# Optimization experiments

Measured on AMD Instinct MI355X. Metric: run time of the kernel, lower is better.

## Reference

```python
import jax, jax.numpy as jnp
import numpy as np

N = 100000
E = 3200000
IN_C, HID_C, OUT_C = 128, 128, 64


def setup_inputs() -> dict:
    key = jax.random.key(0)
    k_x, k_e, k_w1, k_w2 = jax.random.split(key, 4)
    x = jax.random.normal(k_x, (N, IN_C), dtype=jnp.float32)
    edge_index = jax.random.randint(k_e, (2, E), 0, N, dtype=jnp.int64)
    # GCNConv uses Glorot-init weight [in, out] and zero bias
    W1 = jax.random.normal(k_w1, (IN_C, HID_C), dtype=jnp.float32) * (1.0 / np.sqrt(IN_C))
    b1 = jnp.zeros((HID_C,), dtype=jnp.float32)
    W2 = jax.random.normal(k_w2, (HID_C, OUT_C), dtype=jnp.float32) * (1.0 / np.sqrt(HID_C))
    b2 = jnp.zeros((OUT_C,), dtype=jnp.float32)
    return {"x": x, "edge_index": edge_index, "W1": W1, "b1": b1, "W2": W2, "b2": b2}


def _gcn_norm(edge_index, n_nodes):
    """Add self-loops and compute symmetric normalization coefficients."""
    loop = jnp.arange(n_nodes, dtype=edge_index.dtype)
    src = jnp.concatenate([edge_index[0], loop])  # [E+N]
    dst = jnp.concatenate([edge_index[1], loop])  # [E+N]
    ones = jnp.ones(src.shape[0], dtype=jnp.float32)
    deg = jax.ops.segment_sum(ones, dst, num_segments=n_nodes)  # in-degree w/ self loops
    dinv = jnp.where(deg > 0, jax.lax.rsqrt(deg), 0.0)
    norm = dinv[src] * dinv[dst]  # [E+N]
    return src, dst, norm


def _gcn_conv(x, W, b, src, dst, norm, n_nodes):
    h = x @ W                                   # [N, out] dense transform first (PyG order)
    msg = norm[:, None] * h[src]                # gather + scale  [E+N, out]
    out = jax.ops.segment_sum(msg, dst, num_segments=n_nodes)  # scatter-add
    return out + b


def reference(x, edge_index, W1, b1, W2, b2):
    src, dst, norm = _gcn_norm(edge_index, N)
    h = _gcn_conv(x, W1, b1, src, dst, norm, N)
    h = jax.nn.relu(h)
    out = _gcn_conv(h, W2, b2, src, dst, norm, N)
    return out
```

## Files before the change

kernel.cpp:

```cpp
#include <hip/hip_runtime.h>

typedef unsigned int u32;
typedef unsigned short u16;
typedef unsigned long long u64;
typedef __bf16 bf16x8 __attribute__((ext_vector_type(8)));
typedef float floatx4 __attribute__((ext_vector_type(4)));
typedef float floatx2 __attribute__((ext_vector_type(2)));
typedef u32 u32x2 __attribute__((ext_vector_type(2)));
typedef u32 u32x4 __attribute__((ext_vector_type(4)));


__device__ __forceinline__ u16 f2bf(float f) {
  u32 u = __float_as_uint(f);
  u += 0x7fffu + ((u >> 16) & 1u);
  return (u16)(u >> 16);
}
__device__ __forceinline__ float bflo(u32 v) { return __uint_as_float(v << 16); }
__device__ __forceinline__ float bfhi(u32 v) { return __uint_as_float(v & 0xffff0000u); }
__device__ __forceinline__ floatx2 bf2(u32 v) {
  floatx2 r; r.x = bflo(v); r.y = bfhi(v); return r;
}

#define SLICE_SH 10
#define SL (1 << SLICE_SH)
#define MAXNS 128
#define NBBIN 1280

__device__ __forceinline__ void gemm1_body(const float* __restrict__ X,
                                           const float* __restrict__ W,
                                           u16* __restrict__ Y, int nrows,
                                           int bid, u16* Wt) {
  constexpr int K = 128, OUT = 128, NT = 8, LDW = 136;
  int tid = threadIdx.x;
  for (int idx = tid; idx < K * OUT; idx += 256) {
    int k = idx >> 7, n = idx & 127;
    Wt[n * LDW + k] = f2bf(W[idx]);
  }
  __syncthreads();
  int lane = tid & 63, wave = tid >> 6;
  int quad = lane >> 4, low = lane & 15;
  int mBase = bid * 64 + wave * 16;
  int m = mBase + low;
  int ml = (m < nrows) ? m : (nrows - 1);
  floatx4 acc[NT];
#pragma unroll
  for (int i = 0; i < NT; i++) acc[i] = (floatx4)0.0f;
#pragma unroll
  for (int kb = 0; kb < 4; kb++) {
    int k0 = kb * 32 + quad * 8;
    floatx4 p0 = *(const floatx4*)(X + (size_t)ml * K + k0);
    floatx4 p1 = *(const floatx4*)(X + (size_t)ml * K + k0 + 4);
    union { bf16x8 v; u16 s[8]; } au;
#pragma unroll
    for (int j = 0; j < 4; j++) { au.s[j] = f2bf(p0[j]); au.s[4 + j] = f2bf(p1[j]); }
#pragma unroll
    for (int nt = 0; nt < NT; nt++) {
      bf16x8 b = *(const bf16x8*)(&Wt[(nt * 16 + low) * LDW + k0]);
      acc[nt] = __builtin_amdgcn_mfma_f32_16x16x32_bf16(au.v, b, acc[nt], 0, 0, 0);
    }
  }
#pragma unroll
  for (int nt = 0; nt < NT; nt++) {
    int col = nt * 16 + low;
#pragma unroll
    for (int r = 0; r < 4; r++) {
      int row = mBase + quad * 4 + r;
      if (row < nrows) Y[(size_t)row * OUT + col] = f2bf(acc[nt][r]);
    }
  }
}

__device__ __forceinline__ void bin_body(const int* __restrict__ ei,
                                         int* __restrict__ scur,
                                         u64* __restrict__ stA, u64* __restrict__ stB,
                                         int splitS, int cap, int e, int ns,
                                         int bid, int* hist, int* curs) {
  int per = (e + NBBIN - 1) / NBBIN;
  int e0 = bid * per;
  int e1 = e0 + per; if (e1 > e) e1 = e;
  for (int t = threadIdx.x; t < ns; t += 256) hist[t] = 0;
  __syncthreads();
  for (int i = e0 + threadIdx.x; i < e1; i += 256) {
    int d = ei[e + i];
    atomicAdd(&hist[d >> SLICE_SH], 1);
  }
  __syncthreads();
  for (int t = threadIdx.x; t < ns; t += 256)
    curs[t] = atomicAdd(&scur[t], hist[t]);
  __syncthreads();
  int i = e0 + threadIdx.x;
  for (; i + 768 < e1; i += 1024) {
    int d[4], s[4], pos[4];
#pragma unroll
    for (int p = 0; p < 4; p++) {
      int ii = i + 256 * p;
      s[p] = ei[ii]; d[p] = ei[e + ii];
    }
#pragma unroll
    for (int p = 0; p < 4; p++) pos[p] = atomicAdd(&curs[d[p] >> SLICE_SH], 1);
#pragma unroll
    for (int p = 0; p < 4; p++) {
      int sl = d[p] >> SLICE_SH;
      u64* st = (sl < splitS) ? stA + (size_t)sl * cap : stB + (size_t)(sl - splitS) * cap;
      st[pos[p]] = ((u64)(u32)d[p] << 32) | (u32)s[p];
    }
  }
  for (; i < e1; i += 256) {
    int s = ei[i], d = ei[e + i];
    int sl = d >> SLICE_SH;
    u64* st = (sl < splitS) ? stA + (size_t)sl * cap : stB + (size_t)(sl - splitS) * cap;
    st[atomicAdd(&curs[sl], 1)] = ((u64)(u32)d << 32) | (u32)s;
  }
}

__global__ __launch_bounds__(256) void gemm1_bin(const float* __restrict__ X,
                                                 const float* __restrict__ W1,
                                                 u16* __restrict__ Y, int nrows, int nbGemm,
                                                 const int* __restrict__ ei,
                                                 int* __restrict__ scur,
                                                 u64* __restrict__ stA, u64* __restrict__ stB,
                                                 int splitS, int cap, int e, int ns) {
  __shared__ __attribute__((aligned(16))) char smbuf[128 * 136 * 2];
  int id = blockIdx.x;
  int small = (NBBIN < nbGemm) ? NBBIN : nbGemm;
  int isBin, bid;
  if (id < 2 * small) { isBin = !(id & 1); bid = id >> 1; }
  else { bid = small + (id - 2 * small); isBin = (NBBIN > nbGemm); }
  if (isBin) {
    int* hist = (int*)smbuf;
    int* curs = hist + MAXNS;
    bin_body(ei, scur, stA, stB, splitS, cap, e, ns, bid, hist, curs);
  } else {
    gemm1_body(X, W1, Y, nrows, bid, (u16*)smbuf);
  }
}

__global__ __launch_bounds__(1024) void fill_slice3(const u64* __restrict__ stA,
                                                    const u64* __restrict__ stB,
                                                    const int* __restrict__ scur,
                                                    int* __restrict__ rp,
                                                    float* __restrict__ dinv,
                                                    int* __restrict__ csr,
                                                    int splitS, int cap, int n, int ns) {
  __shared__ int cnt[SL];
  __shared__ int part[SL];
  __shared__ int sb[MAXNS];
  const int s = blockIdx.x;
  const int base = s << SLICE_SH;
  const int tid = threadIdx.x;
  cnt[tid] = 0;
  if (tid < MAXNS) sb[tid] = (tid < ns) ? scur[tid] : 0;
  __syncthreads();
  for (int off = 1; off < MAXNS; off <<= 1) {
    int v = 0;
    if (tid < MAXNS && tid >= off) v = sb[tid - off];
    __syncthreads();
    if (tid < MAXNS) sb[tid] += v;
    __syncthreads();
  }
  const int csrLo = s ? sb[s - 1] : 0;
  const int m = sb[s] - csrLo;
  if (s == ns - 1 && tid == 0) rp[n] = sb[ns - 1];
  const u64* st = (s < splitS) ? stA + (size_t)s * cap : stB + (size_t)(s - splitS) * cap;
  {
    int i = tid;
    for (; i + 7168 < m; i += 8192) {
      int b[8];
#pragma unroll
      for (int p = 0; p < 8; p++) b[p] = (int)(st[i + 1024 * p] >> 32) & (SL - 1);
#pragma unroll
      for (int p = 0; p < 8; p++) atomicAdd(&cnt[b[p]], 1);
    }
    for (; i < m; i += 1024)
      atomicAdd(&cnt[(int)(st[i] >> 32) & (SL - 1)], 1);
  }
  __syncthreads();
  int c0 = cnt[tid];
  part[tid] = c0;
  __syncthreads();
  for (int off = 1; off < SL; off <<= 1) {
    int t = (tid >= off) ? part[tid - off] : 0;
    __syncthreads();
    part[tid] += t;
    __syncthreads();
  }
  int p0 = csrLo + (tid ? part[tid - 1] : 0);
  __syncthreads();
  cnt[tid] = p0;
  int d0 = base + tid;
  if (d0 < n) { rp[d0] = p0; dinv[d0] = rsqrtf((float)(c0 + 1)); }
  __syncthreads();
  {
    int i = tid;
    for (; i + 7168 < m; i += 8192) {
      u64 pr[8]; int pos[8];
#pragma unroll
      for (int p = 0; p < 8; p++) pr[p] = st[i + 1024 * p];
#pragma unroll
      for (int p = 0; p < 8; p++)
        pos[p] = atomicAdd(&cnt[(int)(pr[p] >> 32) & (SL - 1)], 1);
#pragma unroll
      for (int p = 0; p < 8; p++) csr[pos[p]] = (int)(pr[p] & 0xffffffffu);
    }
    for (; i < m; i += 1024) {
      u64 pr = st[i];
      int pos = atomicAdd(&cnt[(int)(pr >> 32) & (SL - 1)], 1);
      csr[pos] = (int)(pr & 0xffffffffu);
    }
  }
}

__global__ __launch_bounds__(256) void agg128_g2(const u32* __restrict__ H,
                                                 const int* __restrict__ rp,
                                                 const int* __restrict__ cs,
                                                 const float* __restrict__ dinv,
                                                 const float* __restrict__ b1,
                                                 const float* __restrict__ W2,
                                                 u16* __restrict__ h2, int n) {
  __shared__ u16 Wt[64 * 136];
  __shared__ u16 Arow[16 * 136];
  const int tid = threadIdx.x;
  for (int idx = tid; idx < 128 * 64; idx += 256) {
    int k = idx >> 6, nn = idx & 63;
    Wt[nn * 136 + k] = f2bf(W2[idx]);
  }
  const int nodeBase = blockIdx.x * 4;
  const int wave = tid >> 6, lane = tid & 63;
  int node = nodeBase + wave;
  int nodeC = (node < n) ? node : (n - 1);
  int e4 = lane >> 4, c = lane & 15;
  int s0 = rp[nodeC], s1 = rp[nodeC + 1];
  floatx2 a2[4];
#pragma unroll
  for (int k = 0; k < 4; k++) a2[k] = (floatx2)0.0f;
  for (int base = s0; base < s1; base += 64) {
    int nb = s1 - base; if (nb > 64) nb = 64;
    int src = 0; float dv = 0.f;
    if (lane < nb) { src = cs[base + lane]; dv = dinv[src]; }
    for (int j = 0; j < nb; j += 16) {
      u32x4 v[4]; float w[4];
#pragma unroll
      for (int p = 0; p < 4; p++) {
        int idx = j + 4 * p + e4;
        int sj = __shfl(src, idx);
        w[p] = __shfl(dv, idx);
        v[p] = *(const u32x4*)(H + (size_t)sj * 64 + 4 * c);
      }
#pragma unroll
      for (int p = 0; p < 4; p++) {
        floatx2 wp; wp.x = w[p]; wp.y = w[p];
#pragma unroll
        for (int k = 0; k < 4; k++) {
          a2[k] += wp * bf2(v[p][k]);
        }
      }
    }
  }
#pragma unroll
  for (int k = 0; k < 4; k++) {
    a2[k].x += __shfl_xor(a2[k].x, 16);
    a2[k].y += __shfl_xor(a2[k].y, 16);
    a2[k].x += __shfl_xor(a2[k].x, 32);
    a2[k].y += __shfl_xor(a2[k].y, 32);
  }
  float ds = dinv[nodeC];
  u32x4 vs = *(const u32x4*)(H + (size_t)nodeC * 64 + 4 * c);
  floatx4 bb0 = *(const floatx4*)(b1 + 8 * c);
  floatx4 bb1 = *(const floatx4*)(b1 + 8 * c + 4);
  float r[8];
#pragma unroll
  for (int k = 0; k < 4; k++) {
    r[2 * k]     = ds * (a2[k].x + ds * bflo(vs[k]));
    r[2 * k + 1] = ds * (a2[k].y + ds * bfhi(vs[k]));
  }
#pragma unroll
  for (int k = 0; k < 4; k++) { r[k] += bb0[k]; r[4 + k] += bb1[k]; }
#pragma unroll
  for (int k = 0; k < 8; k++) r[k] = fmaxf(r[k], 0.f);
  if (e4 == 0) {
    union { u16 s[8]; u32x4 v; } pk;
#pragma unroll
    for (int k = 0; k < 8; k++) pk.s[k] = f2bf(r[k]);
    *(u32x4*)&Arow[wave * 136 + 8 * c] = pk.v;
  }
  __syncthreads();
  const int quad = e4, low = c;
  floatx4 acc = (floatx4)0.0f;
#pragma unroll
  for (int kb = 0; kb < 4; kb++) {
    int k0 = kb * 32 + quad * 8;
    bf16x8 af = *(const bf16x8*)&Arow[low * 136 + k0];
    bf16x8 bf = *(const bf16x8*)&Wt[(wave * 16 + low) * 136 + k0];
    acc = __builtin_amdgcn_mfma_f32_16x16x32_bf16(af, bf, acc, 0, 0, 0);
  }
  if (quad == 0) {
#pragma unroll
    for (int rI = 0; rI < 4; rI++) {
      int row = nodeBase + rI;
      if (row < n) h2[(size_t)row * 64 + wave * 16 + low] = f2bf(acc[rI]);
    }
  }
}

__global__ __launch_bounds__(256) void agg_64(const u16* __restrict__ Hu,
                                              const int* __restrict__ rp,
                                              const int* __restrict__ cs,
                                              const float* __restrict__ dinv,
                                              const float* __restrict__ b2,
                                              float* __restrict__ out, int n) {
  const u32* H = (const u32*)Hu;
  int node = blockIdx.x * 4 + (threadIdx.x >> 6);
  if (node >= n) return;
  int lane = threadIdx.x & 63;
  int e4 = lane >> 4, c = lane & 15;
  int s0 = rp[node], s1 = rp[node + 1];
  floatx2 a2[2];
  a2[0] = (floatx2)0.0f; a2[1] = (floatx2)0.0f;
  for (int base = s0; base < s1; base += 64) {
    int nb = s1 - base; if (nb > 64) nb = 64;
    int src = 0; float dv = 0.f;
    if (lane < nb) { src = cs[base + lane]; dv = dinv[src]; }
    for (int j = 0; j < nb; j += 16) {
      u32x2 v[4]; float w[4];
#pragma unroll
      for (int p = 0; p < 4; p++) {
        int idx = j + 4 * p + e4;
        int sj = __shfl(src, idx);
        w[p] = __shfl(dv, idx);
        v[p] = *(const u32x2*)(H + (size_t)sj * 32 + 2 * c);
      }
#pragma unroll
      for (int p = 0; p < 4; p++) {
        floatx2 wp; wp.x = w[p]; wp.y = w[p];
        a2[0] += wp * bf2(v[p].x);
        a2[1] += wp * bf2(v[p].y);
      }
    }
  }
#pragma unroll
  for (int k = 0; k < 2; k++) {
    a2[k].x += __shfl_xor(a2[k].x, 16);
    a2[k].y += __shfl_xor(a2[k].y, 16);
    a2[k].x += __shfl_xor(a2[k].x, 32);
    a2[k].y += __shfl_xor(a2[k].y, 32);
  }
  float ds = dinv[node];
  u32x2 vs = *(const u32x2*)(H + (size_t)node * 32 + 2 * c);
  floatx4 bf = *(const floatx4*)(b2 + 4 * c);
  if (e4 == 0) {
    floatx4 o;
    o[0] = ds * (a2[0].x + ds * bflo(vs.x)) + bf[0];
    o[1] = ds * (a2[0].y + ds * bfhi(vs.x)) + bf[1];
    o[2] = ds * (a2[1].x + ds * bflo(vs.y)) + bf[2];
    o[3] = ds * (a2[1].y + ds * bfhi(vs.y)) + bf[3];
    *(floatx4*)(out + (size_t)node * 64 + 4 * c) = o;
  }
}


extern "C" void kernel_launch(void* const* d_in, const int* in_sizes, int n_in,
                              void* d_out, int out_size, void* d_ws, size_t ws_size,
                              hipStream_t stream) {
  const float* x  = (const float*)d_in[0];
  const int*   ei = (const int*)d_in[1];
  const float* W1 = (const float*)d_in[2];
  const float* b1 = (const float*)d_in[3];
  const float* W2 = (const float*)d_in[4];
  const float* b2 = (const float*)d_in[5];
  const int N = in_sizes[0] / 128;
  const int E = in_sizes[1] / 2;
  const int NS = (N + SL - 1) >> SLICE_SH;

  int CAP = (E + NS - 1) / NS;
  CAP += CAP / 8;
  size_t doutSlots = ((size_t)out_size * 4) / 8;
  int SPLIT = (int)(doutSlots / (size_t)CAP);
  if (SPLIT > NS) SPLIT = NS;

  auto al = [](size_t v) { return (v + 255) & ~(size_t)255; };
  char* ws = (char*)d_ws;
  size_t o = 0;
  int*   scur  = (int*)(ws + o);  o += 512;
  int*   rp    = (int*)(ws + o);  o += al((size_t)(N + 1) * 4);
  float* dinv  = (float*)(ws + o); o += al((size_t)N * 4);
  int*   csr   = (int*)(ws + o);  o += al((size_t)E * 4);
  u16*   h     = (u16*)(ws + o);  o += al((size_t)N * 128 * 2);
  u16*   h2    = (u16*)(ws + o);  o += al((size_t)N * 128 * 2);
  u64* stA = (u64*)d_out;
  u64* stB = (u64*)h2;

  const int nbGemm = (N + 63) / 64;

  hipMemsetAsync(scur, 0, 512, stream);
  gemm1_bin<<<NBBIN + nbGemm, 256, 0, stream>>>(x, W1, h, N, nbGemm,
                                                ei, scur, stA, stB, SPLIT, CAP, E, NS);
  fill_slice3<<<NS, 1024, 0, stream>>>(stA, stB, scur, rp, dinv, csr, SPLIT, CAP, N, NS);
  agg128_g2<<<(N + 3) / 4, 256, 0, stream>>>((const u32*)h, rp, csr, dinv, b1, W2, h2, N);
  agg_64<<<(N + 3) / 4, 256, 0, stream>>>(h2, rp, csr, dinv, b2, (float*)d_out, N);
}
```

Baseline: 382.6 us.

## Pack staged edges into 32-bit words and count degrees during binning

Staged edges are now 32-bit words holding the local destination in the high bits and a 17-bit source in the low bits, instead of 64-bit pairs. This halves staging write and read traffic. Per-node in-degree is counted with global atomics in the binning pass, so the fill kernel no longer makes a separate counting pass over the staged edges. The cost is 3.2M extra global atomics and a larger memset. The packing also only holds while node ids fit in 17 bits (N up to 131072).

```diff
diff --git a/kernel.cpp b/kernel.cpp
--- a/kernel.cpp
+++ b/kernel.cpp
@@ -25,6 +25,7 @@
 #define SL (1 << SLICE_SH)
 #define MAXNS 128
 #define NBBIN 1280
+#define SRC_BITS 17
 
 __device__ __forceinline__ void gemm1_body(const float* __restrict__ X,
                                            const float* __restrict__ W,
@@ -72,7 +73,8 @@
 
 __device__ __forceinline__ void bin_body(const int* __restrict__ ei,
                                          int* __restrict__ scur,
-                                         u64* __restrict__ stA, u64* __restrict__ stB,
+                                         int* __restrict__ deg,
+                                         u32* __restrict__ stA, u32* __restrict__ stB,
                                          int splitS, int cap, int e, int ns,
                                          int bid, int* hist, int* curs) {
   int per = (e + NBBIN - 1) / NBBIN;
@@ -83,6 +85,7 @@
   for (int i = e0 + threadIdx.x; i < e1; i += 256) {
     int d = ei[e + i];
     atomicAdd(&hist[d >> SLICE_SH], 1);
+    atomicAdd(&deg[d], 1);
   }
   __syncthreads();
   for (int t = threadIdx.x; t < ns; t += 256)
@@ -101,15 +104,15 @@
 #pragma unroll
     for (int p = 0; p < 4; p++) {
       int sl = d[p] >> SLICE_SH;
-      u64* st = (sl < splitS) ? stA + (size_t)sl * cap : stB + (size_t)(sl - splitS) * cap;
-      st[pos[p]] = ((u64)(u32)d[p] << 32) | (u32)s[p];
+      u32* st = (sl < splitS) ? stA + (size_t)sl * cap : stB + (size_t)(sl - splitS) * cap;
+      st[pos[p]] = ((u32)(d[p] & (SL - 1)) << SRC_BITS) | (u32)s[p];
     }
   }
   for (; i < e1; i += 256) {
     int s = ei[i], d = ei[e + i];
     int sl = d >> SLICE_SH;
-    u64* st = (sl < splitS) ? stA + (size_t)sl * cap : stB + (size_t)(sl - splitS) * cap;
-    st[atomicAdd(&curs[sl], 1)] = ((u64)(u32)d << 32) | (u32)s;
+    u32* st = (sl < splitS) ? stA + (size_t)sl * cap : stB + (size_t)(sl - splitS) * cap;
+    st[atomicAdd(&curs[sl], 1)] = ((u32)(d & (SL - 1)) << SRC_BITS) | (u32)s;
   }
 }
 
@@ -118,7 +121,8 @@
                                                  u16* __restrict__ Y, int nrows, int nbGemm,
                                                  const int* __restrict__ ei,
                                                  int* __restrict__ scur,
-                                                 u64* __restrict__ stA, u64* __restrict__ stB,
+                                                 int* __restrict__ deg,
+                                                 u32* __restrict__ stA, u32* __restrict__ stB,
                                                  int splitS, int cap, int e, int ns) {
   __shared__ __attribute__((aligned(16))) char smbuf[128 * 136 * 2];
   int id = blockIdx.x;
@@ -129,15 +133,16 @@
   if (isBin) {
     int* hist = (int*)smbuf;
     int* curs = hist + MAXNS;
-    bin_body(ei, scur, stA, stB, splitS, cap, e, ns, bid, hist, curs);
+    bin_body(ei, scur, deg, stA, stB, splitS, cap, e, ns, bid, hist, curs);
   } else {
     gemm1_body(X, W1, Y, nrows, bid, (u16*)smbuf);
   }
 }
 
-__global__ __launch_bounds__(1024) void fill_slice3(const u64* __restrict__ stA,
-                                                    const u64* __restrict__ stB,
+__global__ __launch_bounds__(1024) void fill_slice4(const u32* __restrict__ stA,
+                                                    const u32* __restrict__ stB,
                                                     const int* __restrict__ scur,
+                                                    const int* __restrict__ deg,
                                                     int* __restrict__ rp,
                                                     float* __restrict__ dinv,
                                                     int* __restrict__ csr,
@@ -148,8 +153,9 @@
   const int s = blockIdx.x;
   const int base = s << SLICE_SH;
   const int tid = threadIdx.x;
-  cnt[tid] = 0;
+  const int d0 = base + tid;
   if (tid < MAXNS) sb[tid] = (tid < ns) ? scur[tid] : 0;
+  int c0 = (d0 < n) ? deg[d0] : 0;
   __syncthreads();
   for (int off = 1; off < MAXNS; off <<= 1) {
     int v = 0;
@@ -161,21 +167,6 @@
   const int csrLo = s ? sb[s - 1] : 0;
   const int m = sb[s] - csrLo;
   if (s == ns - 1 && tid == 0) rp[n] = sb[ns - 1];
-  const u64* st = (s < splitS) ? stA + (size_t)s * cap : stB + (size_t)(s - splitS) * cap;
-  {
-    int i = tid;
-    for (; i + 7168 < m; i += 8192) {
-      int b[8];
-#pragma unroll
-      for (int p = 0; p < 8; p++) b[p] = (int)(st[i + 1024 * p] >> 32) & (SL - 1);
-#pragma unroll
-      for (int p = 0; p < 8; p++) atomicAdd(&cnt[b[p]], 1);
-    }
-    for (; i < m; i += 1024)
-      atomicAdd(&cnt[(int)(st[i] >> 32) & (SL - 1)], 1);
-  }
-  __syncthreads();
-  int c0 = cnt[tid];
   part[tid] = c0;
   __syncthreads();
   for (int off = 1; off < SL; off <<= 1) {
@@ -185,27 +176,26 @@
     __syncthreads();
   }
   int p0 = csrLo + (tid ? part[tid - 1] : 0);
-  __syncthreads();
   cnt[tid] = p0;
-  int d0 = base + tid;
   if (d0 < n) { rp[d0] = p0; dinv[d0] = rsqrtf((float)(c0 + 1)); }
   __syncthreads();
+  const u32* st = (s < splitS) ? stA + (size_t)s * cap : stB + (size_t)(s - splitS) * cap;
   {
     int i = tid;
     for (; i + 7168 < m; i += 8192) {
-      u64 pr[8]; int pos[8];
+      u32 pr[8]; int pos[8];
 #pragma unroll
       for (int p = 0; p < 8; p++) pr[p] = st[i + 1024 * p];
 #pragma unroll
       for (int p = 0; p < 8; p++)
-        pos[p] = atomicAdd(&cnt[(int)(pr[p] >> 32) & (SL - 1)], 1);
-#pragma unroll
-      for (int p = 0; p < 8; p++) csr[pos[p]] = (int)(pr[p] & 0xffffffffu);
+        pos[p] = atomicAdd(&cnt[pr[p] >> SRC_BITS], 1);
+#pragma unroll
+      for (int p = 0; p < 8; p++) csr[pos[p]] = (int)(pr[p] & ((1u << SRC_BITS) - 1u));
     }
     for (; i < m; i += 1024) {
-      u64 pr = st[i];
-      int pos = atomicAdd(&cnt[(int)(pr >> 32) & (SL - 1)], 1);
-      csr[pos] = (int)(pr & 0xffffffffu);
+      u32 pr = st[i];
+      int pos = atomicAdd(&cnt[pr >> SRC_BITS], 1);
+      csr[pos] = (int)(pr & ((1u << SRC_BITS) - 1u));
     }
   }
 }
@@ -373,7 +363,7 @@
 
   int CAP = (E + NS - 1) / NS;
   CAP += CAP / 8;
-  size_t doutSlots = ((size_t)out_size * 4) / 8;
+  size_t doutSlots = (size_t)out_size / 4;
   int SPLIT = (int)(doutSlots / (size_t)CAP);
   if (SPLIT > NS) SPLIT = NS;
 
@@ -381,20 +371,23 @@
   char* ws = (char*)d_ws;
   size_t o = 0;
   int*   scur  = (int*)(ws + o);  o += 512;
+  int*   deg   = (int*)(ws + o);  o += al((size_t)N * 4);
+  size_t zeroBytes = o;
   int*   rp    = (int*)(ws + o);  o += al((size_t)(N + 1) * 4);
   float* dinv  = (float*)(ws + o); o += al((size_t)N * 4);
   int*   csr   = (int*)(ws + o);  o += al((size_t)E * 4);
   u16*   h     = (u16*)(ws + o);  o += al((size_t)N * 128 * 2);
   u16*   h2    = (u16*)(ws + o);  o += al((size_t)N * 128 * 2);
-  u64* stA = (u64*)d_out;
-  u64* stB = (u64*)h2;
+  u32* stA = (u32*)d_out;
+  u32* stB = (u32*)h2;
 
   const int nbGemm = (N + 63) / 64;
 
-  hipMemsetAsync(scur, 0, 512, stream);
+  hipMemsetAsync(scur, 0, zeroBytes, stream);
   gemm1_bin<<<NBBIN + nbGemm, 256, 0, stream>>>(x, W1, h, N, nbGemm,
-                                                ei, scur, stA, stB, SPLIT, CAP, E, NS);
-  fill_slice3<<<NS, 1024, 0, stream>>>(stA, stB, scur, rp, dinv, csr, SPLIT, CAP, N, NS);
+                                                ei, scur, deg, stA, stB, SPLIT, CAP, E, NS);
+  fill_slice4<<<NS, 1024, 0, stream>>>(stA, stB, scur, deg, rp, dinv, csr,
+                                       SPLIT, CAP, N, NS);
   agg128_g2<<<(N + 3) / 4, 256, 0, stream>>>((const u32*)h, rp, csr, dinv, b1, W2, h2, N);
   agg_64<<<(N + 3) / 4, 256, 0, stream>>>(h2, rp, csr, dinv, b2, (float*)d_out, N);
 }
```

Measured after the change: 470.8 us. 1.23x slower.
